# Kernel optimization log

Hardware: AMD Instinct MI355X
Metric: run time of the kernel (lower is better)

Reference implementation:

```python
import jax, jax.numpy as jnp
import numpy as np


def floor_ste(x):
    # forward: floor(x); backward: identity (straight-through estimator)
    return x + jax.lax.stop_gradient(jnp.floor(x) - x)


def _int_polynomial(x_int, sf):
    c0, c1, c2 = 0.35815147, 0.96963238, 1.0
    b_int = floor_ste((c1 / c0) / sf)
    c_int = floor_ste((c2 / c0) / (sf * sf))
    z = x_int * (x_int + b_int) + c_int
    return z, c0 * sf * sf


def _int_exp(x_int, sf):
    x0 = -0.69314718
    n = 15
    x0_int = floor_ste(x0 / sf)
    x_int = jnp.maximum(x_int, n * x0_int)
    q = floor_ste(x_int / x0_int)
    r = x_int - x0_int * q
    exp_int, exp_sf = _int_polynomial(r, sf)
    exp_int = jnp.maximum(floor_ste(exp_int * jnp.exp2(n - q)), 0.0)
    return exp_int, exp_sf / (2.0 ** n)


def _int_softmax(x, sf):
    x_int = x / sf
    x_int = x_int - jnp.max(x_int, axis=-1, keepdims=True)
    exp_int, exp_sf = _int_exp(x_int, sf)
    exp_int_sum = jnp.sum(exp_int, axis=-1, keepdims=True)
    return exp_int, exp_int_sum, exp_sf


def setup_inputs() -> dict:
    key = jax.random.key(0)
    k1, = jax.random.split(key, 1)
    x = jax.random.normal(k1, (2, 16, 1024, 1024), dtype=jnp.float32)
    scale = jnp.float32(0.05)          # activation quantization step
    threshold = jnp.array([0.1], dtype=jnp.float32)  # nn.Parameter init
    return {"x": x, "scale": scale, "threshold": threshold}


def reference(x, scale, threshold):
    output_bit = 8
    threshold_bits = 8
    exp_int, exp_int_sum, exp_sf = _int_softmax(x, scale)
    factor = floor_ste((2.0 ** 32) / exp_int_sum)
    out_scale_A = threshold / (2.0 ** output_bit - 1.0)   # shape [1]
    out_scale_B = 1.0 / (2.0 ** output_bit - 1.0)
    approx_threshold = (floor_ste(threshold * 2.0 ** threshold_bits)
                        * exp_int_sum / (2.0 ** threshold_bits))
    mask_A = exp_int <= approx_threshold
    exp_int_A = jnp.where(mask_A, exp_int, 0.0)
    exp_int_B = jnp.where(mask_A, 0.0, exp_int)
    softmax_int_A = floor_ste(exp_int_A * factor / ((2.0 ** 32) * out_scale_A))
    softmax_int_B = floor_ste(exp_int_B * factor / ((2.0 ** 32) * out_scale_B))
    softmax_int_B = jnp.minimum(softmax_int_B, 255.0)
    return softmax_int_A * out_scale_A + softmax_int_B * out_scale_B
```

## Files before the change

kernel.cpp:

```cpp
#include <hip/hip_runtime.h>
#include <math.h>

#pragma clang fp contract(off)

#define TPB 256
#define ROWLEN 1024
#define PERSIST_BLOCKS 2048

typedef float f32x4 __attribute__((ext_vector_type(4)));

static __device__ __forceinline__ float bcast_f32(float v) {
    return __int_as_float(__builtin_amdgcn_readfirstlane(__float_as_int(v)));
}

__device__ __forceinline__ float wave_max_dpp(float m) {
    const int NEG_INF = 0xff800000;
    int v;
    v = __builtin_amdgcn_update_dpp(NEG_INF, __float_as_int(m), 0x111, 0xf, 0xf, false);
    m = fmaxf(m, __int_as_float(v));
    v = __builtin_amdgcn_update_dpp(NEG_INF, __float_as_int(m), 0x112, 0xf, 0xf, false);
    m = fmaxf(m, __int_as_float(v));
    v = __builtin_amdgcn_update_dpp(NEG_INF, __float_as_int(m), 0x114, 0xf, 0xf, false);
    m = fmaxf(m, __int_as_float(v));
    v = __builtin_amdgcn_update_dpp(NEG_INF, __float_as_int(m), 0x118, 0xf, 0xf, false);
    m = fmaxf(m, __int_as_float(v));
    v = __builtin_amdgcn_update_dpp(NEG_INF, __float_as_int(m), 0x142, 0xa, 0xf, false);
    m = fmaxf(m, __int_as_float(v));
    v = __builtin_amdgcn_update_dpp(NEG_INF, __float_as_int(m), 0x143, 0xc, 0xf, false);
    m = fmaxf(m, __int_as_float(v));
    return __int_as_float(__builtin_amdgcn_readlane(__float_as_int(m), 63));
}

__device__ __forceinline__ unsigned wave_sum_dpp_u32(unsigned a) {
    int v;
    v = __builtin_amdgcn_update_dpp(0, (int)a, 0x111, 0xf, 0xf, false); a += (unsigned)v;
    v = __builtin_amdgcn_update_dpp(0, (int)a, 0x112, 0xf, 0xf, false); a += (unsigned)v;
    v = __builtin_amdgcn_update_dpp(0, (int)a, 0x114, 0xf, 0xf, false); a += (unsigned)v;
    v = __builtin_amdgcn_update_dpp(0, (int)a, 0x118, 0xf, 0xf, false); a += (unsigned)v;
    v = __builtin_amdgcn_update_dpp(0, (int)a, 0x142, 0xa, 0xf, false); a += (unsigned)v;
    v = __builtin_amdgcn_update_dpp(0, (int)a, 0x143, 0xc, 0xf, false); a += (unsigned)v;
    return (unsigned)__builtin_amdgcn_readlane((int)a, 63);
}

__global__ __launch_bounds__(TPB, 8) void qsplit_int_softmax_kernel(
    const float* __restrict__ x,
    const float* __restrict__ scale_p,
    const float* __restrict__ thr_p,
    float* __restrict__ out,
    const int rows)
{
    const int tid  = threadIdx.x;
    const int lane = tid & 63;
    const int wid  = tid >> 6;
    const int nw   = (int)(gridDim.x << 2);
    int r = (int)(blockIdx.x << 2) | wid;

    const float sf  = scale_p[0];
    const float thr = thr_p[0];

    const float rh = bcast_f32(1.0f / sf);
    const float er = __builtin_fmaf(-sf, rh, 1.0f);
    const float rl = bcast_f32(rh * er);

    #define DF_DIV(a) ({ float _p = (a) * rh; \
                         float _e = __builtin_fmaf((a), rh, -_p); \
                         _p + __builtin_fmaf((a), rl, _e); })
    const float x0f    = bcast_f32(floorf(DF_DIV(-0.69314718f)));
    const float bfc    = bcast_f32(floorf(DF_DIV(2.7073824f)));
    const float s2     = sf * sf;
    const float r2h    = 1.0f / s2;
    const float r2e    = __builtin_fmaf(-s2, r2h, 1.0f);
    const float r2l    = r2h * r2e;
    const float cq     = __builtin_fmaf(2.7921141f, r2l,
                         2.7921141f * r2h);
    const float cfc    = bcast_f32(floorf(cq));
    const float clampf = bcast_f32(15.0f * x0f);
    const float invx0f = bcast_f32(1.0f / x0f);

    const float osA  = bcast_f32(thr / 255.0f);
    const float osB  = bcast_f32(1.0f / 255.0f);
    const float invA = bcast_f32(1.0f / (4294967296.0f * osA));
    const float invB = bcast_f32(1.0f / (4294967296.0f * osB));
    const float thrq = bcast_f32(floorf(thr * 256.0f));

    if (r >= rows) return;

    const size_t step = (size_t)nw * ROWLEN;
    const float* px = x   + (size_t)r * ROWLEN + ((size_t)lane << 2);
    float*       po = out + (size_t)r * ROWLEN + ((size_t)lane << 2);

    float cur[16];
    #pragma unroll
    for (int g = 0; g < 4; ++g) {
        const f32x4 v = *(const f32x4*)(px + (g << 8));
        cur[4*g+0] = v[0]; cur[4*g+1] = v[1];
        cur[4*g+2] = v[2]; cur[4*g+3] = v[3];
    }

    for (;;) {
        const bool has_next = (r + nw < rows);
        float nxt[16];
        if (has_next) {
            const float* pn = px + step;
            #pragma unroll
            for (int g = 0; g < 4; ++g) {
                const f32x4 v = *(const f32x4*)(pn + (g << 8));
                nxt[4*g+0] = v[0]; nxt[4*g+1] = v[1];
                nxt[4*g+2] = v[2]; nxt[4*g+3] = v[3];
            }
        }

        #pragma unroll
        for (int j = 0; j < 16; ++j) {
            const float xx = cur[j];
            const float p  = xx * rh;
            const float e  = __builtin_fmaf(xx, rh, -p);
            cur[j] = p + __builtin_fmaf(xx, rl, e);
        }

        float t0 = fmaxf(cur[0], cur[1]),  t1 = fmaxf(cur[2], cur[3]);
        float t2 = fmaxf(cur[4], cur[5]),  t3 = fmaxf(cur[6], cur[7]);
        float t4 = fmaxf(cur[8], cur[9]),  t5 = fmaxf(cur[10], cur[11]);
        float t6 = fmaxf(cur[12], cur[13]),t7 = fmaxf(cur[14], cur[15]);
        t0 = fmaxf(t0, t1); t2 = fmaxf(t2, t3);
        t4 = fmaxf(t4, t5); t6 = fmaxf(t6, t7);
        t0 = fmaxf(t0, t2); t4 = fmaxf(t4, t6);
        const float m = wave_max_dpp(fmaxf(t0, t4));

        unsigned usum = 0;
        #pragma unroll
        for (int j = 0; j < 16; ++j) {
            float v = cur[j] - m;
            v = fmaxf(v, clampf);
            const float qf = floorf(v * invx0f);
            const int   qi = (int)qf;
            const float rr = v - x0f * qf;
            const float t  = rr + bfc;
            const float z  = rr * t + cfc;
            float ei = floorf(ldexpf(z, 15 - qi));
            ei = fmaxf(ei, 0.0f);
            cur[j] = ei;
            usum += (unsigned)ei;
        }

        const unsigned lo = wave_sum_dpp_u32(usum & 0xFFFFu);
        const unsigned hi = wave_sum_dpp_u32(usum >> 16);
        const double s = (double)(((unsigned long long)hi << 16) + lo);

        const float fac_f = bcast_f32((float)floor(4294967296.0 / s));
        const float ath_f = bcast_f32((float)(((double)thrq * s) * (1.0 / 256.0)));

        #pragma unroll
        for (int g = 0; g < 4; ++g) {
            f32x4 o;
            #pragma unroll
            for (int jj = 0; jj < 4; ++jj) {
                const float ei  = cur[4*g+jj];
                const bool  isA = (ei <= ath_f);
                const float t1_ = ei * fac_f;
                const float t2_ = t1_ * (isA ? invA : invB);
                float si = floorf(t2_);
                si = fminf(si, isA ? 3.0e38f : 255.0f);
                o[jj] = si * (isA ? osA : osB);
            }
            __builtin_nontemporal_store(o, (f32x4*)(po + (g << 8)));
        }

        if (!has_next) break;
        r  += nw;
        px += step; po += step;
        #pragma unroll
        for (int j = 0; j < 16; ++j) cur[j] = nxt[j];
    }
}

extern "C" void kernel_launch(void* const* d_in, const int* in_sizes, int n_in,
                              void* d_out, int out_size, void* d_ws, size_t ws_size,
                              hipStream_t stream) {
    const float* x     = (const float*)d_in[0];
    const float* scale = (const float*)d_in[1];
    const float* thr   = (const float*)d_in[2];
    float* out = (float*)d_out;

    const int total = in_sizes[0];
    const int rows  = total / ROWLEN;

    const int wave_blocks = (rows + 3) / 4;
    const int blocks = wave_blocks < PERSIST_BLOCKS ? wave_blocks : PERSIST_BLOCKS;

    qsplit_int_softmax_kernel<<<dim3(blocks), dim3(TPB), 0, stream>>>(
        x, scale, thr, out, rows);
}
```

Before: 236.2 us.

## Replace persistent row loop with two interleaved rows per wave, batched reductions

Drops the persistent grid-stride loop with software prefetch. Each wave now handles exactly two rows, with loads, math and DPP reductions interleaved across both rows for more instruction-level parallelism, and the grid is sized to cover all rows. The double-precision division for the scaling factor is replaced by a float reciprocal with a double-checked correction step. It also removes the occupancy hint from launch_bounds, which may change register allocation, and launches many more blocks.

```diff
diff --git a/kernel.cpp b/kernel.cpp
--- a/kernel.cpp
+++ b/kernel.cpp
@@ -5,7 +5,6 @@
 
 #define TPB 256
 #define ROWLEN 1024
-#define PERSIST_BLOCKS 2048
 
 typedef float f32x4 __attribute__((ext_vector_type(4)));
 
@@ -13,36 +12,49 @@
     return __int_as_float(__builtin_amdgcn_readfirstlane(__float_as_int(v)));
 }
 
-__device__ __forceinline__ float wave_max_dpp(float m) {
-    const int NEG_INF = 0xff800000;
-    int v;
-    v = __builtin_amdgcn_update_dpp(NEG_INF, __float_as_int(m), 0x111, 0xf, 0xf, false);
-    m = fmaxf(m, __int_as_float(v));
-    v = __builtin_amdgcn_update_dpp(NEG_INF, __float_as_int(m), 0x112, 0xf, 0xf, false);
-    m = fmaxf(m, __int_as_float(v));
-    v = __builtin_amdgcn_update_dpp(NEG_INF, __float_as_int(m), 0x114, 0xf, 0xf, false);
-    m = fmaxf(m, __int_as_float(v));
-    v = __builtin_amdgcn_update_dpp(NEG_INF, __float_as_int(m), 0x118, 0xf, 0xf, false);
-    m = fmaxf(m, __int_as_float(v));
-    v = __builtin_amdgcn_update_dpp(NEG_INF, __float_as_int(m), 0x142, 0xa, 0xf, false);
-    m = fmaxf(m, __int_as_float(v));
-    v = __builtin_amdgcn_update_dpp(NEG_INF, __float_as_int(m), 0x143, 0xc, 0xf, false);
-    m = fmaxf(m, __int_as_float(v));
-    return __int_as_float(__builtin_amdgcn_readlane(__float_as_int(m), 63));
-}
-
-__device__ __forceinline__ unsigned wave_sum_dpp_u32(unsigned a) {
-    int v;
-    v = __builtin_amdgcn_update_dpp(0, (int)a, 0x111, 0xf, 0xf, false); a += (unsigned)v;
-    v = __builtin_amdgcn_update_dpp(0, (int)a, 0x112, 0xf, 0xf, false); a += (unsigned)v;
-    v = __builtin_amdgcn_update_dpp(0, (int)a, 0x114, 0xf, 0xf, false); a += (unsigned)v;
-    v = __builtin_amdgcn_update_dpp(0, (int)a, 0x118, 0xf, 0xf, false); a += (unsigned)v;
-    v = __builtin_amdgcn_update_dpp(0, (int)a, 0x142, 0xa, 0xf, false); a += (unsigned)v;
-    v = __builtin_amdgcn_update_dpp(0, (int)a, 0x143, 0xc, 0xf, false); a += (unsigned)v;
-    return (unsigned)__builtin_amdgcn_readlane((int)a, 63);
-}
-
-__global__ __launch_bounds__(TPB, 8) void qsplit_int_softmax_kernel(
+__device__ __forceinline__ void wave_max_dpp2(float& a, float& b) {
+    const int NI = 0xff800000;
+    int va, vb;
+#define MSTG(sel, rm, bm) \
+    va = __builtin_amdgcn_update_dpp(NI, __float_as_int(a), sel, rm, bm, false); \
+    vb = __builtin_amdgcn_update_dpp(NI, __float_as_int(b), sel, rm, bm, false); \
+    a = fmaxf(a, __int_as_float(va)); \
+    b = fmaxf(b, __int_as_float(vb));
+    MSTG(0x111,0xf,0xf) MSTG(0x112,0xf,0xf) MSTG(0x114,0xf,0xf)
+    MSTG(0x118,0xf,0xf) MSTG(0x142,0xa,0xf) MSTG(0x143,0xc,0xf)
+#undef MSTG
+    a = __int_as_float(__builtin_amdgcn_readlane(__float_as_int(a), 63));
+    b = __int_as_float(__builtin_amdgcn_readlane(__float_as_int(b), 63));
+}
+
+__device__ __forceinline__ void wave_sum_dpp4(unsigned& a, unsigned& b,
+                                              unsigned& c, unsigned& d) {
+    int v0, v1, v2, v3;
+#define SSTG(sel, rm, bm) \
+    v0 = __builtin_amdgcn_update_dpp(0, (int)a, sel, rm, bm, false); \
+    v1 = __builtin_amdgcn_update_dpp(0, (int)b, sel, rm, bm, false); \
+    v2 = __builtin_amdgcn_update_dpp(0, (int)c, sel, rm, bm, false); \
+    v3 = __builtin_amdgcn_update_dpp(0, (int)d, sel, rm, bm, false); \
+    a += (unsigned)v0; b += (unsigned)v1; c += (unsigned)v2; d += (unsigned)v3;
+    SSTG(0x111,0xf,0xf) SSTG(0x112,0xf,0xf) SSTG(0x114,0xf,0xf)
+    SSTG(0x118,0xf,0xf) SSTG(0x142,0xa,0xf) SSTG(0x143,0xc,0xf)
+#undef SSTG
+    a = (unsigned)__builtin_amdgcn_readlane((int)a, 63);
+    b = (unsigned)__builtin_amdgcn_readlane((int)b, 63);
+    c = (unsigned)__builtin_amdgcn_readlane((int)c, 63);
+    d = (unsigned)__builtin_amdgcn_readlane((int)d, 63);
+}
+
+__device__ __forceinline__ float fac_exact(double s) {
+    const float r0 = __builtin_amdgcn_rcpf((float)s);
+    float qf = floorf(4294967296.0f * r0);
+    const double t = (double)qf * s;
+    if (t > 4294967296.0)           qf -= 1.0f;
+    else if (t + s <= 4294967296.0) qf += 1.0f;
+    return qf;
+}
+
+__global__ __launch_bounds__(TPB) void qsplit_int_softmax_kernel(
     const float* __restrict__ x,
     const float* __restrict__ scale_p,
     const float* __restrict__ thr_p,
@@ -52,8 +64,11 @@
     const int tid  = threadIdx.x;
     const int lane = tid & 63;
     const int wid  = tid >> 6;
-    const int nw   = (int)(gridDim.x << 2);
-    int r = (int)(blockIdx.x << 2) | wid;
+    const int gw   = (int)(blockIdx.x << 2) | wid;
+    const int rA   = gw << 1;
+    if (rA >= rows) return;
+    const int  rB   = rA | 1;
+    const bool hasB = (rB < rows);
 
     const float sf  = scale_p[0];
     const float thr = thr_p[0];
@@ -83,94 +98,117 @@
     const float invB = bcast_f32(1.0f / (4294967296.0f * osB));
     const float thrq = bcast_f32(floorf(thr * 256.0f));
 
-    if (r >= rows) return;
-
-    const size_t step = (size_t)nw * ROWLEN;
-    const float* px = x   + (size_t)r * ROWLEN + ((size_t)lane << 2);
-    float*       po = out + (size_t)r * ROWLEN + ((size_t)lane << 2);
-
-    float cur[16];
+    const float* pA = x + (size_t)rA * ROWLEN + ((size_t)lane << 2);
+    const float* pB = hasB ? (pA + ROWLEN) : pA;
+    float a[16], b[16];
     #pragma unroll
     for (int g = 0; g < 4; ++g) {
-        const f32x4 v = *(const f32x4*)(px + (g << 8));
-        cur[4*g+0] = v[0]; cur[4*g+1] = v[1];
-        cur[4*g+2] = v[2]; cur[4*g+3] = v[3];
-    }
-
-    for (;;) {
-        const bool has_next = (r + nw < rows);
-        float nxt[16];
-        if (has_next) {
-            const float* pn = px + step;
-            #pragma unroll
-            for (int g = 0; g < 4; ++g) {
-                const f32x4 v = *(const f32x4*)(pn + (g << 8));
-                nxt[4*g+0] = v[0]; nxt[4*g+1] = v[1];
-                nxt[4*g+2] = v[2]; nxt[4*g+3] = v[3];
-            }
+        const f32x4 va = *(const f32x4*)(pA + (g << 8));
+        const f32x4 vb = *(const f32x4*)(pB + (g << 8));
+        a[4*g+0]=va[0]; a[4*g+1]=va[1]; a[4*g+2]=va[2]; a[4*g+3]=va[3];
+        b[4*g+0]=vb[0]; b[4*g+1]=vb[1]; b[4*g+2]=vb[2]; b[4*g+3]=vb[3];
+    }
+
+    #pragma unroll
+    for (int j = 0; j < 16; ++j) {
+        { const float xx = a[j];
+          const float p  = xx * rh;
+          const float e  = __builtin_fmaf(xx, rh, -p);
+          a[j] = p + __builtin_fmaf(xx, rl, e); }
+        { const float xx = b[j];
+          const float p  = xx * rh;
+          const float e  = __builtin_fmaf(xx, rh, -p);
+          b[j] = p + __builtin_fmaf(xx, rl, e); }
+    }
+
+    float mA, mB;
+    {
+        float t0 = fmaxf(a[0],a[1]),  t1 = fmaxf(a[2],a[3]);
+        float t2 = fmaxf(a[4],a[5]),  t3 = fmaxf(a[6],a[7]);
+        float t4 = fmaxf(a[8],a[9]),  t5 = fmaxf(a[10],a[11]);
+        float t6 = fmaxf(a[12],a[13]),t7 = fmaxf(a[14],a[15]);
+        t0 = fmaxf(t0,t1); t2 = fmaxf(t2,t3); t4 = fmaxf(t4,t5); t6 = fmaxf(t6,t7);
+        mA = fmaxf(fmaxf(t0,t2), fmaxf(t4,t6));
+    }
+    {
+        float t0 = fmaxf(b[0],b[1]),  t1 = fmaxf(b[2],b[3]);
+        float t2 = fmaxf(b[4],b[5]),  t3 = fmaxf(b[6],b[7]);
+        float t4 = fmaxf(b[8],b[9]),  t5 = fmaxf(b[10],b[11]);
+        float t6 = fmaxf(b[12],b[13]),t7 = fmaxf(b[14],b[15]);
+        t0 = fmaxf(t0,t1); t2 = fmaxf(t2,t3); t4 = fmaxf(t4,t5); t6 = fmaxf(t6,t7);
+        mB = fmaxf(fmaxf(t0,t2), fmaxf(t4,t6));
+    }
+    wave_max_dpp2(mA, mB);
+
+    unsigned usA = 0, usB = 0;
+    #pragma unroll
+    for (int j = 0; j < 16; ++j) {
+        { float v = a[j] - mA;
+          v = fmaxf(v, clampf);
+          const float qf = floorf(v * invx0f);
+          const int   qi = (int)qf;
+          const float rr = v - x0f * qf;
+          const float t  = rr + bfc;
+          const float z  = rr * t + cfc;
+          float ei = floorf(ldexpf(z, 15 - qi));
+          ei = fmaxf(ei, 0.0f);
+          a[j] = ei; usA += (unsigned)ei; }
+        { float v = b[j] - mB;
+          v = fmaxf(v, clampf);
+          const float qf = floorf(v * invx0f);
+          const int   qi = (int)qf;
+          const float rr = v - x0f * qf;
+          const float t  = rr + bfc;
+          const float z  = rr * t + cfc;
+          float ei = floorf(ldexpf(z, 15 - qi));
+          ei = fmaxf(ei, 0.0f);
+          b[j] = ei; usB += (unsigned)ei; }
+    }
+
+    unsigned loA = usA & 0xFFFFu, hiA = usA >> 16;
+    unsigned loB = usB & 0xFFFFu, hiB = usB >> 16;
+    wave_sum_dpp4(loA, hiA, loB, hiB);
+    const double sA = (double)(((unsigned long long)hiA << 16) + loA);
+    const double sB = (double)(((unsigned long long)hiB << 16) + loB);
+
+    const float facA = bcast_f32(fac_exact(sA));
+    const float facB = bcast_f32(fac_exact(sB));
+    const float athA = bcast_f32((float)(((double)thrq * sA) * (1.0 / 256.0)));
+    const float athB = bcast_f32((float)(((double)thrq * sB) * (1.0 / 256.0)));
+
+    float* poA = out + (size_t)rA * ROWLEN + ((size_t)lane << 2);
+    #pragma unroll
+    for (int g = 0; g < 4; ++g) {
+        f32x4 o;
+        #pragma unroll
+        for (int jj = 0; jj < 4; ++jj) {
+            const float ei  = a[4*g+jj];
+            const bool  isA = (ei <= athA);
+            const float t1_ = ei * facA;
+            const float t2_ = t1_ * (isA ? invA : invB);
+            float si = floorf(t2_);
+            si = fminf(si, isA ? 3.0e38f : 255.0f);
+            o[jj] = si * (isA ? osA : osB);
         }
-
-        #pragma unroll
-        for (int j = 0; j < 16; ++j) {
-            const float xx = cur[j];
-            const float p  = xx * rh;
-            const float e  = __builtin_fmaf(xx, rh, -p);
-            cur[j] = p + __builtin_fmaf(xx, rl, e);
-        }
-
-        float t0 = fmaxf(cur[0], cur[1]),  t1 = fmaxf(cur[2], cur[3]);
-        float t2 = fmaxf(cur[4], cur[5]),  t3 = fmaxf(cur[6], cur[7]);
-        float t4 = fmaxf(cur[8], cur[9]),  t5 = fmaxf(cur[10], cur[11]);
-        float t6 = fmaxf(cur[12], cur[13]),t7 = fmaxf(cur[14], cur[15]);
-        t0 = fmaxf(t0, t1); t2 = fmaxf(t2, t3);
-        t4 = fmaxf(t4, t5); t6 = fmaxf(t6, t7);
-        t0 = fmaxf(t0, t2); t4 = fmaxf(t4, t6);
-        const float m = wave_max_dpp(fmaxf(t0, t4));
-
-        unsigned usum = 0;
-        #pragma unroll
-        for (int j = 0; j < 16; ++j) {
-            float v = cur[j] - m;
-            v = fmaxf(v, clampf);
-            const float qf = floorf(v * invx0f);
-            const int   qi = (int)qf;
-            const float rr = v - x0f * qf;
-            const float t  = rr + bfc;
-            const float z  = rr * t + cfc;
-            float ei = floorf(ldexpf(z, 15 - qi));
-            ei = fmaxf(ei, 0.0f);
-            cur[j] = ei;
-            usum += (unsigned)ei;
-        }
-
-        const unsigned lo = wave_sum_dpp_u32(usum & 0xFFFFu);
-        const unsigned hi = wave_sum_dpp_u32(usum >> 16);
-        const double s = (double)(((unsigned long long)hi << 16) + lo);
-
-        const float fac_f = bcast_f32((float)floor(4294967296.0 / s));
-        const float ath_f = bcast_f32((float)(((double)thrq * s) * (1.0 / 256.0)));
-
+        __builtin_nontemporal_store(o, (f32x4*)(poA + (g << 8)));
+    }
+    if (hasB) {
+        float* poB = poA + ROWLEN;
         #pragma unroll
         for (int g = 0; g < 4; ++g) {
             f32x4 o;
             #pragma unroll
             for (int jj = 0; jj < 4; ++jj) {
-                const float ei  = cur[4*g+jj];
-                const bool  isA = (ei <= ath_f);
-                const float t1_ = ei * fac_f;
+                const float ei  = b[4*g+jj];
+                const bool  isA = (ei <= athB);
+                const float t1_ = ei * facB;
                 const float t2_ = t1_ * (isA ? invA : invB);
                 float si = floorf(t2_);
                 si = fminf(si, isA ? 3.0e38f : 255.0f);
                 o[jj] = si * (isA ? osA : osB);
             }
-            __builtin_nontemporal_store(o, (f32x4*)(po + (g << 8)));
+            __builtin_nontemporal_store(o, (f32x4*)(poB + (g << 8)));
         }
-
-        if (!has_next) break;
-        r  += nw;
-        px += step; po += step;
-        #pragma unroll
-        for (int j = 0; j < 16; ++j) cur[j] = nxt[j];
     }
 }
 
@@ -185,8 +223,8 @@
     const int total = in_sizes[0];
     const int rows  = total / ROWLEN;
 
-    const int wave_blocks = (rows + 3) / 4;
-    const int blocks = wave_blocks < PERSIST_BLOCKS ? wave_blocks : PERSIST_BLOCKS;
+    const int waves  = (rows + 1) / 2;
+    const int blocks = (waves + 3) / 4;
 
     qsplit_int_softmax_kernel<<<dim3(blocks), dim3(TPB), 0, stream>>>(
         x, scale, thr, out, rows);
```

Measured after the change: 239.1 us. No clear change (+1.2%).

## Drop persistent prefetch loop, use one row per wave, cheaper factor computation

Applied to the files above, without the earlier changes.

Replaces the persistent grid-stride loop with register prefetch of the next row by a plain one-row-per-wave launch over all rows. It also interleaves the two 16-bit DPP sum reductions and swaps the double-precision division for a float reciprocal with a double-checked correction. The aim is to cut register pressure and the cost of the double divide, and to rely on many resident waves for latency hiding instead of software prefetch. The risk is more block launch and prologue overhead per row, since the constants are recomputed for every row.

```diff
diff --git a/kernel.cpp b/kernel.cpp
--- a/kernel.cpp
+++ b/kernel.cpp
@@ -5,7 +5,6 @@
 
 #define TPB 256
 #define ROWLEN 1024
-#define PERSIST_BLOCKS 2048
 
 typedef float f32x4 __attribute__((ext_vector_type(4)));
 
@@ -14,32 +13,43 @@
 }
 
 __device__ __forceinline__ float wave_max_dpp(float m) {
-    const int NEG_INF = 0xff800000;
+    const int NI = 0xff800000;
     int v;
-    v = __builtin_amdgcn_update_dpp(NEG_INF, __float_as_int(m), 0x111, 0xf, 0xf, false);
+    v = __builtin_amdgcn_update_dpp(NI, __float_as_int(m), 0x111, 0xf, 0xf, false);
     m = fmaxf(m, __int_as_float(v));
-    v = __builtin_amdgcn_update_dpp(NEG_INF, __float_as_int(m), 0x112, 0xf, 0xf, false);
+    v = __builtin_amdgcn_update_dpp(NI, __float_as_int(m), 0x112, 0xf, 0xf, false);
     m = fmaxf(m, __int_as_float(v));
-    v = __builtin_amdgcn_update_dpp(NEG_INF, __float_as_int(m), 0x114, 0xf, 0xf, false);
+    v = __builtin_amdgcn_update_dpp(NI, __float_as_int(m), 0x114, 0xf, 0xf, false);
     m = fmaxf(m, __int_as_float(v));
-    v = __builtin_amdgcn_update_dpp(NEG_INF, __float_as_int(m), 0x118, 0xf, 0xf, false);
+    v = __builtin_amdgcn_update_dpp(NI, __float_as_int(m), 0x118, 0xf, 0xf, false);
     m = fmaxf(m, __int_as_float(v));
-    v = __builtin_amdgcn_update_dpp(NEG_INF, __float_as_int(m), 0x142, 0xa, 0xf, false);
+    v = __builtin_amdgcn_update_dpp(NI, __float_as_int(m), 0x142, 0xa, 0xf, false);
     m = fmaxf(m, __int_as_float(v));
-    v = __builtin_amdgcn_update_dpp(NEG_INF, __float_as_int(m), 0x143, 0xc, 0xf, false);
+    v = __builtin_amdgcn_update_dpp(NI, __float_as_int(m), 0x143, 0xc, 0xf, false);
     m = fmaxf(m, __int_as_float(v));
     return __int_as_float(__builtin_amdgcn_readlane(__float_as_int(m), 63));
 }
 
-__device__ __forceinline__ unsigned wave_sum_dpp_u32(unsigned a) {
-    int v;
-    v = __builtin_amdgcn_update_dpp(0, (int)a, 0x111, 0xf, 0xf, false); a += (unsigned)v;
-    v = __builtin_amdgcn_update_dpp(0, (int)a, 0x112, 0xf, 0xf, false); a += (unsigned)v;
-    v = __builtin_amdgcn_update_dpp(0, (int)a, 0x114, 0xf, 0xf, false); a += (unsigned)v;
-    v = __builtin_amdgcn_update_dpp(0, (int)a, 0x118, 0xf, 0xf, false); a += (unsigned)v;
-    v = __builtin_amdgcn_update_dpp(0, (int)a, 0x142, 0xa, 0xf, false); a += (unsigned)v;
-    v = __builtin_amdgcn_update_dpp(0, (int)a, 0x143, 0xc, 0xf, false); a += (unsigned)v;
-    return (unsigned)__builtin_amdgcn_readlane((int)a, 63);
+__device__ __forceinline__ void wave_sum_dpp2(unsigned& a, unsigned& b) {
+    int v0, v1;
+#define SSTG(sel, rm, bm) \
+    v0 = __builtin_amdgcn_update_dpp(0, (int)a, sel, rm, bm, false); \
+    v1 = __builtin_amdgcn_update_dpp(0, (int)b, sel, rm, bm, false); \
+    a += (unsigned)v0; b += (unsigned)v1;
+    SSTG(0x111,0xf,0xf) SSTG(0x112,0xf,0xf) SSTG(0x114,0xf,0xf)
+    SSTG(0x118,0xf,0xf) SSTG(0x142,0xa,0xf) SSTG(0x143,0xc,0xf)
+#undef SSTG
+    a = (unsigned)__builtin_amdgcn_readlane((int)a, 63);
+    b = (unsigned)__builtin_amdgcn_readlane((int)b, 63);
+}
+
+__device__ __forceinline__ float fac_exact(double s) {
+    const float r0 = __builtin_amdgcn_rcpf((float)s);
+    float qf = floorf(4294967296.0f * r0);
+    const double t = (double)qf * s;
+    if (t > 4294967296.0)           qf -= 1.0f;
+    else if (t + s <= 4294967296.0) qf += 1.0f;
+    return qf;
 }
 
 __global__ __launch_bounds__(TPB, 8) void qsplit_int_softmax_kernel(
@@ -52,8 +62,8 @@
     const int tid  = threadIdx.x;
     const int lane = tid & 63;
     const int wid  = tid >> 6;
-    const int nw   = (int)(gridDim.x << 2);
-    int r = (int)(blockIdx.x << 2) | wid;
+    const int r    = (int)(blockIdx.x << 2) | wid;
+    if (r >= rows) return;
 
     const float sf  = scale_p[0];
     const float thr = thr_p[0];
@@ -83,94 +93,68 @@
     const float invB = bcast_f32(1.0f / (4294967296.0f * osB));
     const float thrq = bcast_f32(floorf(thr * 256.0f));
 
-    if (r >= rows) return;
-
-    const size_t step = (size_t)nw * ROWLEN;
-    const float* px = x   + (size_t)r * ROWLEN + ((size_t)lane << 2);
-    float*       po = out + (size_t)r * ROWLEN + ((size_t)lane << 2);
-
-    float cur[16];
+    const float* px = x + (size_t)r * ROWLEN + ((size_t)lane << 2);
+    float a[16];
     #pragma unroll
     for (int g = 0; g < 4; ++g) {
         const f32x4 v = *(const f32x4*)(px + (g << 8));
-        cur[4*g+0] = v[0]; cur[4*g+1] = v[1];
-        cur[4*g+2] = v[2]; cur[4*g+3] = v[3];
+        a[4*g+0] = v[0]; a[4*g+1] = v[1];
+        a[4*g+2] = v[2]; a[4*g+3] = v[3];
     }
 
-    for (;;) {
-        const bool has_next = (r + nw < rows);
-        float nxt[16];
-        if (has_next) {
-            const float* pn = px + step;
-            #pragma unroll
-            for (int g = 0; g < 4; ++g) {
-                const f32x4 v = *(const f32x4*)(pn + (g << 8));
-                nxt[4*g+0] = v[0]; nxt[4*g+1] = v[1];
-                nxt[4*g+2] = v[2]; nxt[4*g+3] = v[3];
-            }
+    #pragma unroll
+    for (int j = 0; j < 16; ++j) {
+        const float xx = a[j];
+        const float p  = xx * rh;
+        const float e  = __builtin_fmaf(xx, rh, -p);
+        a[j] = p + __builtin_fmaf(xx, rl, e);
+    }
+
+    float t0 = fmaxf(a[0],a[1]),  t1 = fmaxf(a[2],a[3]);
+    float t2 = fmaxf(a[4],a[5]),  t3 = fmaxf(a[6],a[7]);
+    float t4 = fmaxf(a[8],a[9]),  t5 = fmaxf(a[10],a[11]);
+    float t6 = fmaxf(a[12],a[13]),t7 = fmaxf(a[14],a[15]);
+    t0 = fmaxf(t0,t1); t2 = fmaxf(t2,t3); t4 = fmaxf(t4,t5); t6 = fmaxf(t6,t7);
+    const float m = wave_max_dpp(fmaxf(fmaxf(t0,t2), fmaxf(t4,t6)));
+
+    unsigned usum = 0;
+    #pragma unroll
+    for (int j = 0; j < 16; ++j) {
+        float v = a[j] - m;
+        v = fmaxf(v, clampf);
+        const float qf = floorf(v * invx0f);
+        const int   qi = (int)qf;
+        const float rr = v - x0f * qf;
+        const float t  = rr + bfc;
+        const float z  = rr * t + cfc;
+        float ei = floorf(ldexpf(z, 15 - qi));
+        ei = fmaxf(ei, 0.0f);
+        a[j] = ei;
+        usum += (unsigned)ei;
+    }
+
+    unsigned lo = usum & 0xFFFFu, hi = usum >> 16;
+    wave_sum_dpp2(lo, hi);
+    const double s = (double)(((unsigned long long)hi << 16) + lo);
+
+    const float fac_f = bcast_f32(fac_exact(s));
+    const float ath_f = bcast_f32((float)(((double)thrq * s) * (1.0 / 256.0)));
+
+    float* po = out + (size_t)r * ROWLEN + ((size_t)lane << 2);
+    #pragma unroll
+    for (int g = 0; g < 4; ++g) {
+        f32x4 o;
+        #pragma unroll
+        for (int jj = 0; jj < 4; ++jj) {
+            const float ei  = a[4*g+jj];
+            const bool  isA = (ei <= ath_f);
+            const float t1_ = ei * fac_f;
+            const float t2_ = t1_ * (isA ? invA : invB);
+            float si = floorf(t2_);
+            si = fminf(si, isA ? 3.0e38f : 255.0f);
+            o[jj] = si * (isA ? osA : osB);
         }
-
-        #pragma unroll
-        for (int j = 0; j < 16; ++j) {
-            const float xx = cur[j];
-            const float p  = xx * rh;
-            const float e  = __builtin_fmaf(xx, rh, -p);
-            cur[j] = p + __builtin_fmaf(xx, rl, e);
-        }
-
-        float t0 = fmaxf(cur[0], cur[1]),  t1 = fmaxf(cur[2], cur[3]);
-        float t2 = fmaxf(cur[4], cur[5]),  t3 = fmaxf(cur[6], cur[7]);
-        float t4 = fmaxf(cur[8], cur[9]),  t5 = fmaxf(cur[10], cur[11]);
-        float t6 = fmaxf(cur[12], cur[13]),t7 = fmaxf(cur[14], cur[15]);
-        t0 = fmaxf(t0, t1); t2 = fmaxf(t2, t3);
-        t4 = fmaxf(t4, t5); t6 = fmaxf(t6, t7);
-        t0 = fmaxf(t0, t2); t4 = fmaxf(t4, t6);
-        const float m = wave_max_dpp(fmaxf(t0, t4));
-
-        unsigned usum = 0;
-        #pragma unroll
-        for (int j = 0; j < 16; ++j) {
-            float v = cur[j] - m;
-            v = fmaxf(v, clampf);
-            const float qf = floorf(v * invx0f);
-            const int   qi = (int)qf;
-            const float rr = v - x0f * qf;
-            const float t  = rr + bfc;
-            const float z  = rr * t + cfc;
-            float ei = floorf(ldexpf(z, 15 - qi));
-            ei = fmaxf(ei, 0.0f);
-            cur[j] = ei;
-            usum += (unsigned)ei;
-        }
-
-        const unsigned lo = wave_sum_dpp_u32(usum & 0xFFFFu);
-        const unsigned hi = wave_sum_dpp_u32(usum >> 16);
-        const double s = (double)(((unsigned long long)hi << 16) + lo);
-
-        const float fac_f = bcast_f32((float)floor(4294967296.0 / s));
-        const float ath_f = bcast_f32((float)(((double)thrq * s) * (1.0 / 256.0)));
-
-        #pragma unroll
-        for (int g = 0; g < 4; ++g) {
-            f32x4 o;
-            #pragma unroll
-            for (int jj = 0; jj < 4; ++jj) {
-                const float ei  = cur[4*g+jj];
-                const bool  isA = (ei <= ath_f);
-                const float t1_ = ei * fac_f;
-                const float t2_ = t1_ * (isA ? invA : invB);
-                float si = floorf(t2_);
-                si = fminf(si, isA ? 3.0e38f : 255.0f);
-                o[jj] = si * (isA ? osA : osB);
-            }
-            __builtin_nontemporal_store(o, (f32x4*)(po + (g << 8)));
-        }
-
-        if (!has_next) break;
-        r  += nw;
-        px += step; po += step;
-        #pragma unroll
-        for (int j = 0; j < 16; ++j) cur[j] = nxt[j];
+        __builtin_nontemporal_store(o, (f32x4*)(po + (g << 8)));
     }
 }
 
@@ -185,8 +169,7 @@
     const int total = in_sizes[0];
     const int rows  = total / ROWLEN;
 
-    const int wave_blocks = (rows + 3) / 4;
-    const int blocks = wave_blocks < PERSIST_BLOCKS ? wave_blocks : PERSIST_BLOCKS;
+    const int blocks = (rows + 3) / 4;
 
     qsplit_int_softmax_kernel<<<dim3(blocks), dim3(TPB), 0, stream>>>(
         x, scale, thr, out, rows);
```

Measured after the change: 233.8 us. No clear change (-1.0%).
